# Performance work log

Hardware: AMD Instinct MI355X
Metric: run time of the kernel (lower is better)

## Reference

```python
import jax, jax.numpy as jnp
import numpy as np
import math

B, D = 4096, 2048  # batch, input_size == hidden_size


def setup_inputs() -> dict:
    key = jax.random.key(0)
    ks = jax.random.split(key, 9)
    stdv = 1.0 / math.sqrt(D)
    u = lambda k, shp: jax.random.uniform(k, shp, jnp.float32, -stdv, stdv)
    return {
        "inputs": jax.random.normal(ks[0], (B, D), jnp.float32),
        "frac_n": jax.random.normal(ks[1], (B, D), jnp.float32),
        "frac_d": jax.random.uniform(ks[2], (B, D), jnp.float32, 0.1, 1.0),
        "scale": jax.random.normal(ks[3], (B, D), jnp.float32),
        "w_r": u(ks[4], (D, D)),
        "w_k": u(ks[5], (D, D)),
        "w_v": u(ks[6], (D, D)),
        "w_o": u(ks[7], (D, D)),
        "w_u": jnp.ones((D,), jnp.float32),  # init.ones_ for 1-D params
        "w_w": jnp.ones((D,), jnp.float32),
    }


def reference(inputs, frac_n, frac_d, scale, w_r, w_k, w_v, w_o, w_u, w_w):
    # r/k/v projections: [B,D] @ [D,D]^T
    r_t = jax.nn.sigmoid(inputs @ w_r.T)
    k_t = inputs @ w_k.T
    v_t = inputs @ w_v.T

    # stabilized WKV update (output path, includes bonus w_u)
    softmax_scale = jnp.maximum(scale, w_u + k_t)
    cell_mult = jnp.exp(scale - softmax_scale)
    attn_mult = jnp.exp(w_u + k_t - softmax_scale)
    frac_n_t = cell_mult * frac_n + attn_mult * v_t
    frac_d_t = cell_mult * frac_d + attn_mult

    # state update path (decay w_w, no bonus)
    next_scale = jnp.maximum(scale + w_w, k_t)
    next_cell_mult = jnp.exp(scale + w_w - next_scale)
    next_attn_mult = jnp.exp(k_t - next_scale)
    next_frac_n = next_cell_mult * frac_n + next_attn_mult * v_t
    next_frac_d = next_cell_mult * frac_d + next_attn_mult

    output = (r_t * (frac_n_t / frac_d_t)) @ w_o.T
    return (output, next_frac_n, next_frac_d, next_scale)
```

## Files before the change

### kernel.cpp

```cpp
#include <hip/hip_runtime.h>
#include <hip/hip_bf16.h>
#include <stdint.h>

#define B_SZ 4096
#define D_SZ 2048

typedef __attribute__((ext_vector_type(4))) float f32x4;
typedef __attribute__((ext_vector_type(8))) __bf16 bf16x8;
typedef __attribute__((ext_vector_type(4))) unsigned short u16x4;
typedef unsigned short u16;

static constexpr long BD = (long)B_SZ * D_SZ;
static constexpr long DD = (long)D_SZ * D_SZ;

__device__ __forceinline__ u16 f2bf(float f) {
  union { float f; unsigned int u; } c; c.f = f;
  unsigned int u = c.u;
  u = (u + 0x7fffu + ((u >> 16) & 1u)) >> 16;
  return (u16)u;
}

__global__ __launch_bounds__(256) void k_convert(
    const float* __restrict__ x,  const float* __restrict__ wr,
    const float* __restrict__ wk, const float* __restrict__ wv,
    const float* __restrict__ wo,
    u16* __restrict__ Xb, u16* __restrict__ W3b, u16* __restrict__ Wob) {
  long i = ((long)blockIdx.x * 256 + threadIdx.x) * 4;
  const float* src; u16* dst; long so, dofs;
  if (i < BD)               { src = x;  so = i;            dst = Xb;  dofs = so; }
  else if (i < BD + DD)     { src = wr; so = i - BD;       dst = W3b; dofs = i - BD; }
  else if (i < BD + 2*DD)   { src = wk; so = i - BD - DD;  dst = W3b; dofs = i - BD; }
  else if (i < BD + 3*DD)   { src = wv; so = i - BD - 2*DD; dst = W3b; dofs = i - BD; }
  else                      { src = wo; so = i - BD - 3*DD; dst = Wob; dofs = so; }
  f32x4 v = *reinterpret_cast<const f32x4*>(src + so);
  u16x4 o;
  o[0] = f2bf(v[0]); o[1] = f2bf(v[1]); o[2] = f2bf(v[2]); o[3] = f2bf(v[3]);
  *reinterpret_cast<u16x4*>(dst + dofs) = o;
}

__device__ __forceinline__ void gload16(const u16* g, const u16* l) {
  __builtin_amdgcn_global_load_lds(
      (const __attribute__((address_space(1))) unsigned int*)g,
      (__attribute__((address_space(3))) unsigned int*)l, 16, 0, 0);
}

#define FENCE asm volatile("" ::: "memory")
#define BAR do { FENCE; __builtin_amdgcn_s_barrier(); FENCE; } while (0)
#define VMC(n) asm volatile("s_waitcnt vmcnt(" #n ")" ::: "memory")

__global__ __launch_bounds__(512, 4) void k_fused(
    const u16* __restrict__ A, const u16* __restrict__ W3,
    const float* __restrict__ frac_n, const float* __restrict__ frac_d,
    const float* __restrict__ scale,
    const float* __restrict__ w_u, const float* __restrict__ w_w,
    float* __restrict__ o_nfn, float* __restrict__ o_nfd,
    float* __restrict__ o_ns,  u16* __restrict__ ab) {
  __shared__ __align__(16) u16 lds[40960];
  const int tid = threadIdx.x;
  const int l   = tid & 63;
  const int wid = tid >> 6;
  const int wm  = wid >> 2;
  const int wn  = wid & 3;
  const int bm = blockIdx.y, bn = blockIdx.x;
  const int K  = D_SZ;
  const int NT = K >> 6;

  const int gcol = (((l & 7) ^ (l >> 3)) << 3);
  const u16* Abase = A + (long)(bm * 128 + wid * 16 + (l >> 3)) * K + gcol;
  const int i0 = wid * 3;

  #define STAGE(t) do {                                                        \
    const long _ko = (long)(t) * 64;                                           \
    u16* _b = &lds[((t) & 1) * 20480];                                         \
    gload16(Abase + _ko,                _b + wid * 1024);                      \
    gload16(Abase + 8 * (long)K + _ko,  _b + wid * 1024 + 512);                \
    _Pragma("unroll")                                                          \
    for (int _c = 0; _c < 3; ++_c) {                                           \
      const int _i = i0 + _c, _j = _i >> 3, _rc = _i & 7;                      \
      const u16* _g = W3 + (long)_j * DD                                       \
                    + (long)(bn * 64 + _rc * 8 + (l >> 3)) * K + gcol + _ko;   \
      gload16(_g, _b + 8192 + _j * 4096 + _rc * 512);                          \
    }                                                                          \
  } while (0)

  const int rby  = (l & 15) * 128;
  const int obx0 = ((l >> 4) * 16) ^ ((l & 7) << 4);
  const int lo0  = (rby + obx0) >> 1;
  const int lo1  = lo0 ^ 32;

  f32x4 acc[3][4] = {};

  auto COMPUTE = [&](int p) {
    const int base = p * 20480;
#pragma unroll
    for (int ks = 0; ks < 2; ++ks) {
      const int lo = ks ? lo1 : lo0;
      bf16x8 af[4], fb[3];
#pragma unroll
      for (int mi = 0; mi < 4; ++mi)
        af[mi] = *reinterpret_cast<const bf16x8*>(
            &lds[base + wm * 4096 + mi * 1024 + lo]);
#pragma unroll
      for (int j = 0; j < 3; ++j)
        fb[j] = *reinterpret_cast<const bf16x8*>(
            &lds[base + 8192 + j * 4096 + wn * 1024 + lo]);
      __builtin_amdgcn_s_setprio(1);
#pragma unroll
      for (int j = 0; j < 3; ++j)
#pragma unroll
        for (int mi = 0; mi < 4; ++mi)
          acc[j][mi] = __builtin_amdgcn_mfma_f32_16x16x32_bf16(
              af[mi], fb[j], acc[j][mi], 0, 0, 0);
      __builtin_amdgcn_s_setprio(0);
    }
  };

  STAGE(0);
  VMC(0); BAR;
  for (int t = 0; t < NT - 1; ++t) {
    STAGE(t + 1);
    COMPUTE(t & 1);
    VMC(0); BAR;
  }
  COMPUTE((NT - 1) & 1);
  #undef STAGE

  const long row0 = (long)bm * 128 + wm * 64 + (l >> 4) * 4;
  const long gc   = (long)bn * 64 + wn * 16 + (l & 15);
  const float wuv = w_u[gc];
  const float wwv = w_w[gc];
#pragma unroll
  for (int mi = 0; mi < 4; ++mi)
#pragma unroll
    for (int r = 0; r < 4; ++r) {
      const long gr  = row0 + mi * 16 + r;
      const long idx = gr * D_SZ + gc;
      const float rr = acc[0][mi][r];
      const float kk = acc[1][mi][r];
      const float vv = acc[2][mi][r];
      const float n  = frac_n[idx];
      const float dn = frac_d[idx];
      const float s  = scale[idx];

      const float rt  = 1.0f / (1.0f + __expf(-rr));
      const float ss  = fmaxf(s, wuv + kk);
      const float cm  = __expf(s - ss);
      const float am  = __expf(wuv + kk - ss);
      const float fnt = cm * n + am * vv;
      const float fdt = cm * dn + am;

      const float ns2 = fmaxf(s + wwv, kk);
      const float ncm = __expf(s + wwv - ns2);
      const float nam = __expf(kk - ns2);

      o_nfn[idx] = ncm * n + nam * vv;
      o_nfd[idx] = ncm * dn + nam;
      o_ns[idx]  = ns2;
      ab[idx]    = f2bf(rt * (fnt / fdt));
    }
}

template <bool OUT_BF16>
__global__ __launch_bounds__(256, 4) void k_gemm128(
    const u16* __restrict__ A, const u16* __restrict__ Bm,
    void* __restrict__ C, int M, int N, int K) {
  __shared__ __align__(16) u16 lds[32768];
  const int tid = threadIdx.x;
  const int l   = tid & 63;
  const int w   = tid >> 6;
  const int wm  = w >> 1, wn = w & 1;
  const int bm = blockIdx.y, bn = blockIdx.x;
  const int NT = K >> 6;

  const int gcol  = (((l & 7) ^ (l >> 3)) << 3);
  const int grow  = w * 32 + (l >> 3);
  const u16* Abase = A  + (long)(bm * 128 + grow) * K + gcol;
  const u16* Bbase = Bm + (long)(bn * 128 + grow) * K + gcol;
  const int sdst = w * 2048;

  #define STAGE(t) do {                                              \
    const long _ko = (long)(t) * 64;                                 \
    u16* _da = &lds[((t) & 1) * 16384 + sdst];                       \
    u16* _db = _da + 8192;                                           \
    _Pragma("unroll")                                                \
    for (int _c = 0; _c < 4; ++_c) {                                 \
      gload16(Abase + (long)_c * 8 * K + _ko, _da + _c * 512);       \
      gload16(Bbase + (long)_c * 8 * K + _ko, _db + _c * 512);       \
    }                                                                \
  } while (0)

  const int rby  = (l & 15) * 128;
  const int obx0 = ((l >> 4) * 16) ^ ((l & 7) << 4);
  const int lo0  = (rby + obx0) >> 1;
  const int lo1  = lo0 ^ 32;

  f32x4 acc[4][4] = {};

  auto COMPUTE = [&](int p) {
#pragma unroll
    for (int ks = 0; ks < 2; ++ks) {
      const int lo = ks ? lo1 : lo0;
      bf16x8 af[4], bf[4];
#pragma unroll
      for (int mi = 0; mi < 4; ++mi)
        af[mi] = *reinterpret_cast<const bf16x8*>(
            &lds[p * 16384 + (wm * 4 + mi) * 1024 + lo]);
#pragma unroll
      for (int ni = 0; ni < 4; ++ni)
        bf[ni] = *reinterpret_cast<const bf16x8*>(
            &lds[p * 16384 + 8192 + (wn * 4 + ni) * 1024 + lo]);
      __builtin_amdgcn_s_setprio(1);
#pragma unroll
      for (int mi = 0; mi < 4; ++mi)
#pragma unroll
        for (int ni = 0; ni < 4; ++ni)
          acc[mi][ni] = __builtin_amdgcn_mfma_f32_16x16x32_bf16(
              af[mi], bf[ni], acc[mi][ni], 0, 0, 0);
      __builtin_amdgcn_s_setprio(0);
    }
  };

  STAGE(0);
  VMC(0); BAR;
  for (int t = 0; t < NT - 1; ++t) {
    STAGE(t + 1);
    COMPUTE(t & 1);
    VMC(0); BAR;
  }
  COMPUTE((NT - 1) & 1);
  #undef STAGE

  const int rb = (l >> 4) * 4, cb = l & 15;
  const long Crow0 = (long)bm * 128 + wm * 64 + rb;
  const long Ccol0 = (long)bn * 128 + wn * 64 + cb;
#pragma unroll
  for (int mi = 0; mi < 4; ++mi)
#pragma unroll
    for (int ni = 0; ni < 4; ++ni)
#pragma unroll
      for (int r = 0; r < 4; ++r) {
        const long gr = Crow0 + mi * 16 + r;
        const long gc = Ccol0 + ni * 16;
        if constexpr (OUT_BF16)
          ((u16*)C)[gr * N + gc] = f2bf(acc[mi][ni][r]);
        else
          ((float*)C)[gr * N + gc] = acc[mi][ni][r];
      }
}

extern "C" void kernel_launch(void* const* d_in, const int* in_sizes, int n_in,
                              void* d_out, int out_size, void* d_ws, size_t ws_size,
                              hipStream_t stream) {
  const float* x      = (const float*)d_in[0];
  const float* frac_n = (const float*)d_in[1];
  const float* frac_d = (const float*)d_in[2];
  const float* scale  = (const float*)d_in[3];
  const float* wr     = (const float*)d_in[4];
  const float* wk     = (const float*)d_in[5];
  const float* wv     = (const float*)d_in[6];
  const float* wo     = (const float*)d_in[7];
  const float* wu     = (const float*)d_in[8];
  const float* ww     = (const float*)d_in[9];
  float* out = (float*)d_out;

  u16* Xb   = (u16*)d_ws;
  u16* W3b  = Xb + BD;
  u16* Wob  = W3b + 3 * DD;
  u16* ab   = Wob + DD;

  {
    const long total = BD + 4 * DD;
    const int blocks = (int)(total / 4 / 256);
    k_convert<<<blocks, 256, 0, stream>>>(x, wr, wk, wv, wo, Xb, W3b, Wob);
  }
  k_fused<<<dim3(D_SZ / 64, B_SZ / 128), 512, 0, stream>>>(
      Xb, W3b, frac_n, frac_d, scale, wu, ww,
      out + BD, out + 2 * BD, out + 3 * BD, ab);
  k_gemm128<false><<<dim3(D_SZ / 128, B_SZ / 128), 256, 0, stream>>>(
      ab, Wob, out, B_SZ, D_SZ, D_SZ);
}
```

Before: 198.7 us.

## Shrink fused r/k/v GEMM tile to 128x32 with 4-wave blocks and K=32 steps

Restructures the fused r/k/v projection kernel from 512-thread blocks with a 128x64 output tile per gate and 64-wide K stages to 256-thread blocks with a 128x32 tile and 32-wide K stages. LDS use drops from about 80KB to 28KB per block and the grid doubles in the N dimension, so more blocks can be resident and more blocks are available to spread across CUs. It also rewrites the LDS swizzle and the fragment offsets to match the new layout. In exchange, each block reuses A across fewer columns, so A traffic doubles, and each K step now has a barrier for half as much MFMA work.

```diff
diff --git a/kernel.cpp b/kernel.cpp
--- a/kernel.cpp
+++ b/kernel.cpp
@@ -48,71 +48,73 @@
 #define BAR do { FENCE; __builtin_amdgcn_s_barrier(); FENCE; } while (0)
 #define VMC(n) asm volatile("s_waitcnt vmcnt(" #n ")" ::: "memory")
 
-__global__ __launch_bounds__(512, 4) void k_fused(
+__global__ __launch_bounds__(256, 4) void k_fused32(
     const u16* __restrict__ A, const u16* __restrict__ W3,
     const float* __restrict__ frac_n, const float* __restrict__ frac_d,
     const float* __restrict__ scale,
     const float* __restrict__ w_u, const float* __restrict__ w_w,
     float* __restrict__ o_nfn, float* __restrict__ o_nfd,
     float* __restrict__ o_ns,  u16* __restrict__ ab) {
-  __shared__ __align__(16) u16 lds[40960];
+  __shared__ __align__(16) u16 lds[14336];
   const int tid = threadIdx.x;
   const int l   = tid & 63;
-  const int wid = tid >> 6;
-  const int wm  = wid >> 2;
-  const int wn  = wid & 3;
+  const int w   = tid >> 6;
+  const int wm  = w >> 1;
+  const int wn  = w & 1;
   const int bm = blockIdx.y, bn = blockIdx.x;
   const int K  = D_SZ;
-  const int NT = K >> 6;
-
-  const int gcol = (((l & 7) ^ (l >> 3)) << 3);
-  const u16* Abase = A + (long)(bm * 128 + wid * 16 + (l >> 3)) * K + gcol;
-  const int i0 = wid * 3;
-
-  #define STAGE(t) do {                                                        \
-    const long _ko = (long)(t) * 64;                                           \
-    u16* _b = &lds[((t) & 1) * 20480];                                         \
-    gload16(Abase + _ko,                _b + wid * 1024);                      \
-    gload16(Abase + 8 * (long)K + _ko,  _b + wid * 1024 + 512);                \
-    _Pragma("unroll")                                                          \
-    for (int _c = 0; _c < 3; ++_c) {                                           \
-      const int _i = i0 + _c, _j = _i >> 3, _rc = _i & 7;                      \
-      const u16* _g = W3 + (long)_j * DD                                       \
-                    + (long)(bn * 64 + _rc * 8 + (l >> 3)) * K + gcol + _ko;   \
-      gload16(_g, _b + 8192 + _j * 4096 + _rc * 512);                          \
-    }                                                                          \
+  const int NT = K >> 5;
+
+  const int gcol = (((l & 3) ^ ((l >> 3) & 3)) << 3);
+  const int srow = l >> 2;
+  const u16* Ab = A  + (long)(bm * 128 + srow) * K + gcol;
+  const u16* Bg = W3 + (long)(bn * 32  + srow) * K + gcol;
+  const int j0 = w >> 1, c0 = w & 1;
+
+  #define STAGE(t) do {                                                       \
+    const long _ko = (long)(t) * 32;                                          \
+    u16* _b = &lds[((t) & 1) * 7168];                                         \
+    gload16(Ab + (long)w * 16 * K + _ko,       _b + w * 512);                 \
+    gload16(Ab + (long)(w + 4) * 16 * K + _ko, _b + (w + 4) * 512);           \
+    gload16(Bg + (long)j0 * DD + (long)c0 * 16 * K + _ko,                     \
+            _b + 4096 + j0 * 1024 + c0 * 512);                                \
+    if (w < 2)                                                                \
+      gload16(Bg + 2L * DD + (long)w * 16 * K + _ko,                          \
+              _b + 4096 + 2048 + w * 512);                                    \
   } while (0)
 
-  const int rby  = (l & 15) * 128;
-  const int obx0 = ((l >> 4) * 16) ^ ((l & 7) << 4);
-  const int lo0  = (rby + obx0) >> 1;
-  const int lo1  = lo0 ^ 32;
+  const int fr = l & 15;
+  const int sl = l >> 4;
+  int offA[4], offB;
+#pragma unroll
+  for (int mi = 0; mi < 4; ++mi) {
+    const int r = wm * 64 + mi * 16 + fr;
+    offA[mi] = r * 32 + ((sl ^ ((r >> 1) & 3)) << 3);
+  }
+  {
+    const int r = wn * 16 + fr;
+    offB = r * 32 + ((sl ^ ((r >> 1) & 3)) << 3);
+  }
 
   f32x4 acc[3][4] = {};
 
   auto COMPUTE = [&](int p) {
-    const int base = p * 20480;
-#pragma unroll
-    for (int ks = 0; ks < 2; ++ks) {
-      const int lo = ks ? lo1 : lo0;
-      bf16x8 af[4], fb[3];
+    const int base = p * 7168;
+    bf16x8 af[4], fb[3];
+#pragma unroll
+    for (int mi = 0; mi < 4; ++mi)
+      af[mi] = *reinterpret_cast<const bf16x8*>(&lds[base + offA[mi]]);
+#pragma unroll
+    for (int j = 0; j < 3; ++j)
+      fb[j] = *reinterpret_cast<const bf16x8*>(&lds[base + 4096 + j * 1024 + offB]);
+    __builtin_amdgcn_s_setprio(1);
+#pragma unroll
+    for (int j = 0; j < 3; ++j)
 #pragma unroll
       for (int mi = 0; mi < 4; ++mi)
-        af[mi] = *reinterpret_cast<const bf16x8*>(
-            &lds[base + wm * 4096 + mi * 1024 + lo]);
-#pragma unroll
-      for (int j = 0; j < 3; ++j)
-        fb[j] = *reinterpret_cast<const bf16x8*>(
-            &lds[base + 8192 + j * 4096 + wn * 1024 + lo]);
-      __builtin_amdgcn_s_setprio(1);
-#pragma unroll
-      for (int j = 0; j < 3; ++j)
-#pragma unroll
-        for (int mi = 0; mi < 4; ++mi)
-          acc[j][mi] = __builtin_amdgcn_mfma_f32_16x16x32_bf16(
-              af[mi], fb[j], acc[j][mi], 0, 0, 0);
-      __builtin_amdgcn_s_setprio(0);
-    }
+        acc[j][mi] = __builtin_amdgcn_mfma_f32_16x16x32_bf16(
+            af[mi], fb[j], acc[j][mi], 0, 0, 0);
+    __builtin_amdgcn_s_setprio(0);
   };
 
   STAGE(0);
@@ -126,7 +128,7 @@
   #undef STAGE
 
   const long row0 = (long)bm * 128 + wm * 64 + (l >> 4) * 4;
-  const long gc   = (long)bn * 64 + wn * 16 + (l & 15);
+  const long gc   = (long)bn * 32 + wn * 16 + (l & 15);
   const float wuv = w_u[gc];
   const float wwv = w_w[gc];
 #pragma unroll
@@ -273,7 +275,7 @@
     const int blocks = (int)(total / 4 / 256);
     k_convert<<<blocks, 256, 0, stream>>>(x, wr, wk, wv, wo, Xb, W3b, Wob);
   }
-  k_fused<<<dim3(D_SZ / 64, B_SZ / 128), 512, 0, stream>>>(
+  k_fused32<<<dim3(D_SZ / 32, B_SZ / 128), 256, 0, stream>>>(
       Xb, W3b, frac_n, frac_d, scale, wu, ww,
       out + BD, out + 2 * BD, out + 3 * BD, ab);
   k_gemm128<false><<<dim3(D_SZ / 128, B_SZ / 128), 256, 0, stream>>>(
```

Result: slower. 255.1 us (+28.4%).

## Retile output GEMM to 128x64 tiles with 32-wide K steps and smaller LDS

Applied to the files above, without the earlier changes.

Replaces the 128x128x64 output-projection GEMM with a 128x64 tile and a 32-element K step. The LDS buffer shrinks from 64KB to 24KB and the LDS swizzle and fragment offsets are rewritten. This doubles the grid to 1024 blocks for better CU fill and occupancy on the second GEMM. The cost is lower arithmetic intensity per block and twice as many barrier iterations per tile.

```diff
diff --git a/kernel.cpp b/kernel.cpp
--- a/kernel.cpp
+++ b/kernel.cpp
@@ -160,64 +160,64 @@
     }
 }
 
-template <bool OUT_BF16>
-__global__ __launch_bounds__(256, 4) void k_gemm128(
+__global__ __launch_bounds__(256, 4) void k_gemm_s(
     const u16* __restrict__ A, const u16* __restrict__ Bm,
-    void* __restrict__ C, int M, int N, int K) {
-  __shared__ __align__(16) u16 lds[32768];
+    float* __restrict__ C, int M, int N, int K) {
+  __shared__ __align__(16) u16 lds[12288];
   const int tid = threadIdx.x;
   const int l   = tid & 63;
   const int w   = tid >> 6;
-  const int wm  = w >> 1, wn = w & 1;
+  const int wm  = w >> 1;
+  const int wn  = w & 1;
   const int bm = blockIdx.y, bn = blockIdx.x;
-  const int NT = K >> 6;
-
-  const int gcol  = (((l & 7) ^ (l >> 3)) << 3);
-  const int grow  = w * 32 + (l >> 3);
-  const u16* Abase = A  + (long)(bm * 128 + grow) * K + gcol;
-  const u16* Bbase = Bm + (long)(bn * 128 + grow) * K + gcol;
-  const int sdst = w * 2048;
-
-  #define STAGE(t) do {                                              \
-    const long _ko = (long)(t) * 64;                                 \
-    u16* _da = &lds[((t) & 1) * 16384 + sdst];                       \
-    u16* _db = _da + 8192;                                           \
-    _Pragma("unroll")                                                \
-    for (int _c = 0; _c < 4; ++_c) {                                 \
-      gload16(Abase + (long)_c * 8 * K + _ko, _da + _c * 512);       \
-      gload16(Bbase + (long)_c * 8 * K + _ko, _db + _c * 512);       \
-    }                                                                \
+  const int NT = K >> 5;
+
+  const int gcol = (((l & 3) ^ ((l >> 3) & 3)) << 3);
+  const int srow = l >> 2;
+  const u16* Ab = A  + (long)(bm * 128 + srow) * K + gcol;
+  const u16* Bb = Bm + (long)(bn * 64  + srow) * K + gcol;
+
+  #define STAGE(t) do {                                                \
+    const long _ko = (long)(t) * 32;                                   \
+    u16* _b = &lds[((t) & 1) * 6144];                                  \
+    gload16(Ab + (long)w * 16 * K + _ko,       _b + w * 512);          \
+    gload16(Ab + (long)(w + 4) * 16 * K + _ko, _b + (w + 4) * 512);    \
+    gload16(Bb + (long)w * 16 * K + _ko,       _b + 4096 + w * 512);   \
   } while (0)
 
-  const int rby  = (l & 15) * 128;
-  const int obx0 = ((l >> 4) * 16) ^ ((l & 7) << 4);
-  const int lo0  = (rby + obx0) >> 1;
-  const int lo1  = lo0 ^ 32;
-
-  f32x4 acc[4][4] = {};
+  const int fr = l & 15;
+  const int sl = l >> 4;
+  int offA[4], offB[2];
+#pragma unroll
+  for (int mi = 0; mi < 4; ++mi) {
+    const int r = wm * 64 + mi * 16 + fr;
+    offA[mi] = r * 32 + ((sl ^ ((r >> 1) & 3)) << 3);
+  }
+#pragma unroll
+  for (int ni = 0; ni < 2; ++ni) {
+    const int r = wn * 32 + ni * 16 + fr;
+    offB[ni] = r * 32 + ((sl ^ ((r >> 1) & 3)) << 3);
+  }
+
+  f32x4 acc[4][2] = {};
 
   auto COMPUTE = [&](int p) {
-#pragma unroll
-    for (int ks = 0; ks < 2; ++ks) {
-      const int lo = ks ? lo1 : lo0;
-      bf16x8 af[4], bf[4];
-#pragma unroll
-      for (int mi = 0; mi < 4; ++mi)
-        af[mi] = *reinterpret_cast<const bf16x8*>(
-            &lds[p * 16384 + (wm * 4 + mi) * 1024 + lo]);
-#pragma unroll
-      for (int ni = 0; ni < 4; ++ni)
-        bf[ni] = *reinterpret_cast<const bf16x8*>(
-            &lds[p * 16384 + 8192 + (wn * 4 + ni) * 1024 + lo]);
-      __builtin_amdgcn_s_setprio(1);
-#pragma unroll
-      for (int mi = 0; mi < 4; ++mi)
-#pragma unroll
-        for (int ni = 0; ni < 4; ++ni)
-          acc[mi][ni] = __builtin_amdgcn_mfma_f32_16x16x32_bf16(
-              af[mi], bf[ni], acc[mi][ni], 0, 0, 0);
-      __builtin_amdgcn_s_setprio(0);
-    }
+    const int base = p * 6144;
+    bf16x8 af[4], bf[2];
+#pragma unroll
+    for (int mi = 0; mi < 4; ++mi)
+      af[mi] = *reinterpret_cast<const bf16x8*>(&lds[base + offA[mi]]);
+#pragma unroll
+    for (int ni = 0; ni < 2; ++ni)
+      bf[ni] = *reinterpret_cast<const bf16x8*>(&lds[base + 4096 + offB[ni]]);
+    __builtin_amdgcn_s_setprio(1);
+#pragma unroll
+    for (int mi = 0; mi < 4; ++mi)
+#pragma unroll
+      for (int ni = 0; ni < 2; ++ni)
+        acc[mi][ni] = __builtin_amdgcn_mfma_f32_16x16x32_bf16(
+            af[mi], bf[ni], acc[mi][ni], 0, 0, 0);
+    __builtin_amdgcn_s_setprio(0);
   };
 
   STAGE(0);
@@ -230,22 +230,15 @@
   COMPUTE((NT - 1) & 1);
   #undef STAGE
 
-  const int rb = (l >> 4) * 4, cb = l & 15;
-  const long Crow0 = (long)bm * 128 + wm * 64 + rb;
-  const long Ccol0 = (long)bn * 128 + wn * 64 + cb;
+  const long Crow0 = (long)bm * 128 + wm * 64 + (l >> 4) * 4;
+  const long Ccol0 = (long)bn * 64 + wn * 32 + (l & 15);
 #pragma unroll
   for (int mi = 0; mi < 4; ++mi)
 #pragma unroll
-    for (int ni = 0; ni < 4; ++ni)
-#pragma unroll
-      for (int r = 0; r < 4; ++r) {
-        const long gr = Crow0 + mi * 16 + r;
-        const long gc = Ccol0 + ni * 16;
-        if constexpr (OUT_BF16)
-          ((u16*)C)[gr * N + gc] = f2bf(acc[mi][ni][r]);
-        else
-          ((float*)C)[gr * N + gc] = acc[mi][ni][r];
-      }
+    for (int ni = 0; ni < 2; ++ni)
+#pragma unroll
+      for (int r = 0; r < 4; ++r)
+        C[(Crow0 + mi * 16 + r) * N + Ccol0 + ni * 16] = acc[mi][ni][r];
 }
 
 extern "C" void kernel_launch(void* const* d_in, const int* in_sizes, int n_in,
@@ -276,6 +269,6 @@
   k_fused<<<dim3(D_SZ / 64, B_SZ / 128), 512, 0, stream>>>(
       Xb, W3b, frac_n, frac_d, scale, wu, ww,
       out + BD, out + 2 * BD, out + 3 * BD, ab);
-  k_gemm128<false><<<dim3(D_SZ / 128, B_SZ / 128), 256, 0, stream>>>(
+  k_gemm_s<<<dim3(D_SZ / 64, B_SZ / 128), 256, 0, stream>>>(
       ab, Wob, out, B_SZ, D_SZ, D_SZ);
 }
```

Result: slower. 220.0 us (+10.7%).

## Fuse input fp32-to-bf16 conversion into fused GEMM A-tile loading

Applied to the files above, without the earlier changes.

Removes the separate conversion pass over the activation matrix; the fused kernel now loads fp32 inputs into registers, packs them to bf16 with v_cvt_pk_bf16_f32, and writes swizzled tiles to LDS. Weights are still converted by a smaller pre-pass. This eliminates a full read/write of the bf16 activation copy but doubles per-block A-operand global traffic and replaces asynchronous global-to-LDS loads with a register round trip and extra waits in the main loop.

```diff
diff --git a/kernel.cpp b/kernel.cpp
--- a/kernel.cpp
+++ b/kernel.cpp
@@ -8,6 +8,7 @@
 typedef __attribute__((ext_vector_type(4))) float f32x4;
 typedef __attribute__((ext_vector_type(8))) __bf16 bf16x8;
 typedef __attribute__((ext_vector_type(4))) unsigned short u16x4;
+typedef __attribute__((ext_vector_type(4))) unsigned int u32x4;
 typedef unsigned short u16;
 
 static constexpr long BD = (long)B_SZ * D_SZ;
@@ -20,18 +21,16 @@
   return (u16)u;
 }
 
-__global__ __launch_bounds__(256) void k_convert(
-    const float* __restrict__ x,  const float* __restrict__ wr,
-    const float* __restrict__ wk, const float* __restrict__ wv,
-    const float* __restrict__ wo,
-    u16* __restrict__ Xb, u16* __restrict__ W3b, u16* __restrict__ Wob) {
+__global__ __launch_bounds__(256) void k_convert_w(
+    const float* __restrict__ wr, const float* __restrict__ wk,
+    const float* __restrict__ wv, const float* __restrict__ wo,
+    u16* __restrict__ W3b, u16* __restrict__ Wob) {
   long i = ((long)blockIdx.x * 256 + threadIdx.x) * 4;
   const float* src; u16* dst; long so, dofs;
-  if (i < BD)               { src = x;  so = i;            dst = Xb;  dofs = so; }
-  else if (i < BD + DD)     { src = wr; so = i - BD;       dst = W3b; dofs = i - BD; }
-  else if (i < BD + 2*DD)   { src = wk; so = i - BD - DD;  dst = W3b; dofs = i - BD; }
-  else if (i < BD + 3*DD)   { src = wv; so = i - BD - 2*DD; dst = W3b; dofs = i - BD; }
-  else                      { src = wo; so = i - BD - 3*DD; dst = Wob; dofs = so; }
+  if (i < DD)          { src = wr; so = i;          dst = W3b; dofs = i; }
+  else if (i < 2 * DD) { src = wk; so = i - DD;     dst = W3b; dofs = i; }
+  else if (i < 3 * DD) { src = wv; so = i - 2 * DD; dst = W3b; dofs = i; }
+  else                 { src = wo; so = i - 3 * DD; dst = Wob; dofs = so; }
   f32x4 v = *reinterpret_cast<const f32x4*>(src + so);
   u16x4 o;
   o[0] = f2bf(v[0]); o[1] = f2bf(v[1]); o[2] = f2bf(v[2]); o[3] = f2bf(v[3]);
@@ -47,9 +46,16 @@
 #define FENCE asm volatile("" ::: "memory")
 #define BAR do { FENCE; __builtin_amdgcn_s_barrier(); FENCE; } while (0)
 #define VMC(n) asm volatile("s_waitcnt vmcnt(" #n ")" ::: "memory")
+#define LGKM0 asm volatile("s_waitcnt lgkmcnt(0)" ::: "memory")
+
+__device__ __forceinline__ unsigned cvtpk(float lo, float hi) {
+  unsigned r;
+  asm("v_cvt_pk_bf16_f32 %0, %1, %2" : "=v"(r) : "v"(lo), "v"(hi));
+  return r;
+}
 
 __global__ __launch_bounds__(512, 4) void k_fused(
-    const u16* __restrict__ A, const u16* __restrict__ W3,
+    const float* __restrict__ X, const u16* __restrict__ W3,
     const float* __restrict__ frac_n, const float* __restrict__ frac_d,
     const float* __restrict__ scale,
     const float* __restrict__ w_u, const float* __restrict__ w_w,
@@ -65,15 +71,34 @@
   const int K  = D_SZ;
   const int NT = K >> 6;
 
+  const float* xg = X + (long)(bm * 128 + wid * 16 + (l >> 3)) * K + (l & 7) * 8;
+  const int awoff = (wid * 16 + (l >> 3)) * 64 + (((l & 7) ^ ((l >> 3) & 7)) << 3);
+
+  f32x4 a0, a1, a2, a3;
+  #define ALOAD(t) do {                                         \
+    const float* _g = xg + (long)(t) * 64;                      \
+    a0 = *reinterpret_cast<const f32x4*>(_g);                   \
+    a1 = *reinterpret_cast<const f32x4*>(_g + 4);               \
+    a2 = *reinterpret_cast<const f32x4*>(_g + 8 * (long)K);     \
+    a3 = *reinterpret_cast<const f32x4*>(_g + 8 * (long)K + 4); \
+  } while (0)
+
+  #define AWRITE(t) do {                                        \
+    u16* _b = &lds[((t) & 1) * 20480];                          \
+    u32x4 w0, w1;                                               \
+    w0[0] = cvtpk(a0[0], a0[1]); w0[1] = cvtpk(a0[2], a0[3]);   \
+    w0[2] = cvtpk(a1[0], a1[1]); w0[3] = cvtpk(a1[2], a1[3]);   \
+    w1[0] = cvtpk(a2[0], a2[1]); w1[1] = cvtpk(a2[2], a2[3]);   \
+    w1[2] = cvtpk(a3[0], a3[1]); w1[3] = cvtpk(a3[2], a3[3]);   \
+    *reinterpret_cast<u32x4*>(&_b[awoff])       = w0;           \
+    *reinterpret_cast<u32x4*>(&_b[awoff + 512]) = w1;           \
+  } while (0)
+
   const int gcol = (((l & 7) ^ (l >> 3)) << 3);
-  const u16* Abase = A + (long)(bm * 128 + wid * 16 + (l >> 3)) * K + gcol;
   const int i0 = wid * 3;
-
-  #define STAGE(t) do {                                                        \
+  #define STAGE_B(t) do {                                                      \
     const long _ko = (long)(t) * 64;                                           \
     u16* _b = &lds[((t) & 1) * 20480];                                         \
-    gload16(Abase + _ko,                _b + wid * 1024);                      \
-    gload16(Abase + 8 * (long)K + _ko,  _b + wid * 1024 + 512);                \
     _Pragma("unroll")                                                          \
     for (int _c = 0; _c < 3; ++_c) {                                           \
       const int _i = i0 + _c, _j = _i >> 3, _rc = _i & 7;                      \
@@ -115,15 +140,20 @@
     }
   };
 
-  STAGE(0);
-  VMC(0); BAR;
+  ALOAD(0); STAGE_B(0);
+  VMC(0); AWRITE(0); LGKM0; BAR;
+
   for (int t = 0; t < NT - 1; ++t) {
-    STAGE(t + 1);
+    ALOAD(t + 1); STAGE_B(t + 1);
     COMPUTE(t & 1);
-    VMC(0); BAR;
+    VMC(0);
+    AWRITE(t + 1);
+    LGKM0; BAR;
   }
   COMPUTE((NT - 1) & 1);
-  #undef STAGE
+  #undef ALOAD
+  #undef AWRITE
+  #undef STAGE_B
 
   const long row0 = (long)bm * 128 + wm * 64 + (l >> 4) * 4;
   const long gc   = (long)bn * 64 + wn * 16 + (l & 15);
@@ -263,18 +293,17 @@
   const float* ww     = (const float*)d_in[9];
   float* out = (float*)d_out;
 
-  u16* Xb   = (u16*)d_ws;
-  u16* W3b  = Xb + BD;
+  u16* W3b  = (u16*)d_ws;
   u16* Wob  = W3b + 3 * DD;
   u16* ab   = Wob + DD;
 
   {
-    const long total = BD + 4 * DD;
+    const long total = 4 * DD;
     const int blocks = (int)(total / 4 / 256);
-    k_convert<<<blocks, 256, 0, stream>>>(x, wr, wk, wv, wo, Xb, W3b, Wob);
+    k_convert_w<<<blocks, 256, 0, stream>>>(wr, wk, wv, wo, W3b, Wob);
   }
   k_fused<<<dim3(D_SZ / 64, B_SZ / 128), 512, 0, stream>>>(
-      Xb, W3b, frac_n, frac_d, scale, wu, ww,
+      x, W3b, frac_n, frac_d, scale, wu, ww,
       out + BD, out + 2 * BD, out + 3 * BD, ab);
   k_gemm128<false><<<dim3(D_SZ / 128, B_SZ / 128), 256, 0, stream>>>(
       ab, Wob, out, B_SZ, D_SZ, D_SZ);
```

Result: slower. 220.4 us (+10.9%).
